# Optimization experiments

Measured on AMD Instinct MI355X. Metric: run time of the kernel, lower is better.

The kernel has to match this reference:

```python
import jax, jax.numpy as jnp
import numpy as np
from jax import lax

J2 = -1.0
J4 = 0.5
KT = 0.5
DT = 0.01
SIGMA = float(np.sqrt(2.0 * KT * DT))  # noise scale per Euler-Maruyama step


def setup_inputs() -> dict:
    key = jax.random.key(0)
    k_x, = jax.random.split(key, 1)
    n_samples, n_dim = 2048, 256
    x0 = jax.random.normal(k_x, (n_samples, n_dim), dtype=jnp.float32)
    b = jnp.zeros((n_dim,), dtype=jnp.float32)  # learned bias parameter
    return {"x0": x0, "b": b, "n_steps": 500}


def reference(x0, b, n_steps):
    # Langevin dynamics: x <- x - grad_V(x)*dt + sqrt(2 kT dt)*N(0,1)
    # grad_V(x) = 2*J2*x + 4*J4*x^3 + b
    keys = jax.random.split(jax.random.key(1), n_steps)

    def step(x, k):
        grad = 2.0 * J2 * x + 4.0 * J4 * x * x * x + b
        noise = jax.random.normal(k, x.shape, x.dtype) * SIGMA
        return x - grad * DT + noise, None

    x, _ = lax.scan(step, x0, keys)
    return x
```

## Files before the change

kernel.cpp:

```cpp
#include <hip/hip_runtime.h>


typedef float v2f __attribute__((ext_vector_type(2)));

__device__ __forceinline__ void tf2x32(unsigned k0, unsigned k1,
                                       unsigned c0, unsigned c1,
                                       unsigned& o0, unsigned& o1) {
  const unsigned k2 = k0 ^ k1 ^ 0x1BD11BDAu;
  unsigned x0 = c0 + k0, x1 = c1 + k1;
#define TF1(R) x0 += x1; x1 = ((x1 << (R)) | (x1 >> (32 - (R)))); x1 ^= x0;
  TF1(13) TF1(15) TF1(26) TF1(6)  x0 += k1; x1 += k2 + 1u;
  TF1(17) TF1(29) TF1(16) TF1(24) x0 += k2; x1 += k0 + 2u;
  TF1(13) TF1(15) TF1(26) TF1(6)  x0 += k0; x1 += k1 + 3u;
  TF1(17) TF1(29) TF1(16) TF1(24) x0 += k1; x1 += k2 + 4u;
  TF1(13) TF1(15) TF1(26) TF1(6)  x0 += k2; x1 += k0 + 5u;
#undef TF1
  o0 = x0; o1 = x1;
}

__device__ __forceinline__ void tf_fold2k(unsigned ka0, unsigned ka1,
                                          unsigned kb0, unsigned kb1,
                                          unsigned cj,
                                          unsigned& ra, unsigned& rb) {
  const unsigned ka2 = ka0 ^ ka1 ^ 0x1BD11BDAu;
  const unsigned kb2 = kb0 ^ kb1 ^ 0x1BD11BDAu;
  unsigned a0 = ka0, a1 = cj + ka1;
  unsigned b0 = kb0, b1 = cj + kb1;
#define TFR2(R)                                   \
  a0 += a1; b0 += b1;                             \
  a1 = ((a1 << (R)) | (a1 >> (32 - (R)))) ^ a0;   \
  b1 = ((b1 << (R)) | (b1 >> (32 - (R)))) ^ b0;
  TFR2(13) TFR2(15) TFR2(26) TFR2(6)
  a0 += ka1; b0 += kb1; a1 += ka2 + 1u; b1 += kb2 + 1u;
  TFR2(17) TFR2(29) TFR2(16) TFR2(24)
  a0 += ka2; b0 += kb2; a1 += ka0 + 2u; b1 += kb0 + 2u;
  TFR2(13) TFR2(15) TFR2(26) TFR2(6)
  a0 += ka0; b0 += kb0; a1 += ka1 + 3u; b1 += kb1 + 3u;
  TFR2(17) TFR2(29) TFR2(16) TFR2(24)
  a0 += ka1; b0 += kb1; a1 += ka2 + 4u; b1 += kb2 + 4u;
  TFR2(13) TFR2(15) TFR2(26) TFR2(6)
  a0 += ka2; b0 += kb2; a1 += ka0 + 5u; b1 += kb0 + 5u;
#undef TFR2
  ra = a0 ^ a1;
  rb = b0 ^ b1;
}

__device__ __forceinline__ void b2n2(unsigned bba, unsigned bbb,
                                     float& na, float& nb) {
  v2f f;
  f.x = __uint_as_float((bba >> 9) | 0x3F800000u) - 1.0f;
  f.y = __uint_as_float((bbb >> 9) | 0x3F800000u) - 1.0f;
  const v2f u = __builtin_elementwise_fma(f, (v2f)2.0f, (v2f)(-0.99999994f));
  const v2f m = u * u;
  const v2f tt = (v2f)1.0f - m;
  v2f l;
  l.x = __log2f(tt.x);
  l.y = __log2f(tt.y);
  const v2f w = l * (v2f)(-0.693147180559945f);
  const bool sa = w.x < 5.0f, sb = w.y < 5.0f;
  const v2f zc = w - (v2f)2.5f;
  v2f z;
  z.x = sa ? zc.x : (__builtin_amdgcn_sqrtf(w.x) - 3.0f);
  z.y = sb ? zc.y : (__builtin_amdgcn_sqrtf(w.y) - 3.0f);
#define SEL2(A, B) (v2f){sa ? (A) : (B), sb ? (A) : (B)}
  v2f p = SEL2(2.81022636e-08f, -0.000200214257f);
  p = __builtin_elementwise_fma(p, z, SEL2(3.43273939e-07f, 0.000100950558f));
  p = __builtin_elementwise_fma(p, z, SEL2(-3.5233877e-06f, 0.00134934322f));
  p = __builtin_elementwise_fma(p, z, SEL2(-4.39150654e-06f, -0.00367342844f));
  p = __builtin_elementwise_fma(p, z, SEL2(0.00021858087f, 0.00573950773f));
  p = __builtin_elementwise_fma(p, z, SEL2(-0.00125372503f, -0.0076224613f));
  p = __builtin_elementwise_fma(p, z, SEL2(-0.00417768164f, 0.00943887047f));
  p = __builtin_elementwise_fma(p, z, SEL2(0.246640727f, 1.00167406f));
  p = __builtin_elementwise_fma(p, z, SEL2(1.50140941f, 2.83297682f));
#undef SEL2
  const v2f n = (p * u) * (v2f)__uint_as_float(0x3FB504F3u);
  na = n.x;
  nb = n.y;
}

__global__ __launch_bounds__(128, 8) void langevin_tf(
    const float* __restrict__ x0p, const float* __restrict__ bias,
    const int* __restrict__ nsteps_p, float* __restrict__ out,
    int N, int ndim) {
  __shared__ __align__(16) unsigned skeys[512 * 2];
  const int n_steps = __builtin_amdgcn_readfirstlane(nsteps_p[0]);
  const int nfill = n_steps < 512 ? n_steps : 512;
  for (int l = (int)threadIdx.x; l < nfill; l += (int)blockDim.x) {
    unsigned o0, o1;
    tf2x32(0u, 1u, 0u, (unsigned)l, o0, o1);
    skeys[2 * l] = o0;
    skeys[2 * l + 1] = o1;
  }
  __syncthreads();

  const int j = (int)(blockIdx.x * blockDim.x + threadIdx.x);
  if (j >= N) return;
  const unsigned cj = (unsigned)j;
  float x = x0p[j];
  const float b = bias[j % ndim];

  if (n_steps <= 512) {
    const uint4* sk4 = (const uint4*)skeys;
    int t = 0;
#pragma unroll 1
    for (; t + 1 < n_steps; t += 2) {
      const uint4 kk = sk4[t >> 1];
      unsigned ra, rb;
      tf_fold2k(kk.x, kk.y, kk.z, kk.w, cj, ra, rb);
      float na, nb;
      b2n2(ra, rb, na, nb);
      float g = -2.0f * x + ((2.0f * x) * x) * x + b;
      x = (x - g * 0.01f) + na * 0.1f;
      g = -2.0f * x + ((2.0f * x) * x) * x + b;
      x = (x - g * 0.01f) + nb * 0.1f;
    }
    if (t < n_steps) {
      const unsigned o0 = skeys[2 * t], o1 = skeys[2 * t + 1];
      unsigned ra, rb;
      tf_fold2k(o0, o1, o0, o1, cj, ra, rb);
      float na, nb;
      b2n2(ra, ra, na, nb);
      const float g = -2.0f * x + ((2.0f * x) * x) * x + b;
      x = (x - g * 0.01f) + na * 0.1f;
    }
  } else {
    for (int t = 0; t < n_steps; t += 2) {
      unsigned oa0, oa1, ob0, ob1;
      tf2x32(0u, 1u, 0u, (unsigned)t, oa0, oa1);
      tf2x32(0u, 1u, 0u, (unsigned)(t + 1), ob0, ob1);
      unsigned ra, rb;
      tf_fold2k(oa0, oa1, ob0, ob1, cj, ra, rb);
      float na, nb;
      b2n2(ra, rb, na, nb);
      float g = -2.0f * x + ((2.0f * x) * x) * x + b;
      x = (x - g * 0.01f) + na * 0.1f;
      if (t + 1 < n_steps) {
        g = -2.0f * x + ((2.0f * x) * x) * x + b;
        x = (x - g * 0.01f) + nb * 0.1f;
      }
    }
  }
  out[j] = x;
}

extern "C" void kernel_launch(void* const* d_in, const int* in_sizes, int n_in,
                              void* d_out, int out_size, void* d_ws, size_t ws_size,
                              hipStream_t stream) {
  (void)n_in; (void)d_ws; (void)ws_size; (void)out_size;
  const float* x0 = (const float*)d_in[0];
  const float* b = (const float*)d_in[1];
  const int* ns = (const int*)d_in[2];
  float* out = (float*)d_out;

  const int n = in_sizes[0];
  const int ndim = in_sizes[1];
  const int block = 128;
  const int grid = (n + block - 1) / block;
  hipLaunchKernelGGL(langevin_tf, dim3(grid), dim3(block), 0, stream,
                     x0, b, ns, out, n, ndim);
}
```

Before: 681.6 us.

## Precompute key schedule, branch tail polynomial wave-uniformly, fold update into FMAs

Stores the third Threefry key word in the shared key table so it is not recomputed per step. The inverse-erf tail polynomial is now evaluated only when some lane in the wave needs it. The gradient update is folded into a chain of FMAs with scalarized constants, and the block size grows to 256. Dropping explicit packed v2f math and the small numeric reordering may cost packed-FMA throughput or add slight differences in rounding.

```diff
diff --git a/kernel.cpp b/kernel.cpp
--- a/kernel.cpp
+++ b/kernel.cpp
@@ -1,7 +1,9 @@
 #include <hip/hip_runtime.h>
 
 
-typedef float v2f __attribute__((ext_vector_type(2)));
+__device__ __forceinline__ float sconst(float v) {
+  return __uint_as_float(__builtin_amdgcn_readfirstlane(__float_as_uint(v)));
+}
 
 __device__ __forceinline__ void tf2x32(unsigned k0, unsigned k1,
                                        unsigned c0, unsigned c1,
@@ -18,78 +20,40 @@
   o0 = x0; o1 = x1;
 }
 
-__device__ __forceinline__ void tf_fold2k(unsigned ka0, unsigned ka1,
-                                          unsigned kb0, unsigned kb1,
-                                          unsigned cj,
+__device__ __forceinline__ void tf_fold2k(uint4 ka, uint4 kb, unsigned cj,
                                           unsigned& ra, unsigned& rb) {
-  const unsigned ka2 = ka0 ^ ka1 ^ 0x1BD11BDAu;
-  const unsigned kb2 = kb0 ^ kb1 ^ 0x1BD11BDAu;
-  unsigned a0 = ka0, a1 = cj + ka1;
-  unsigned b0 = kb0, b1 = cj + kb1;
+  unsigned a0 = ka.x, a1 = cj + ka.y;
+  unsigned b0 = kb.x, b1 = cj + kb.y;
 #define TFR2(R)                                   \
   a0 += a1; b0 += b1;                             \
   a1 = ((a1 << (R)) | (a1 >> (32 - (R)))) ^ a0;   \
   b1 = ((b1 << (R)) | (b1 >> (32 - (R)))) ^ b0;
   TFR2(13) TFR2(15) TFR2(26) TFR2(6)
-  a0 += ka1; b0 += kb1; a1 += ka2 + 1u; b1 += kb2 + 1u;
+  a0 += ka.y; b0 += kb.y; a1 = a1 + ka.z + 1u; b1 = b1 + kb.z + 1u;
   TFR2(17) TFR2(29) TFR2(16) TFR2(24)
-  a0 += ka2; b0 += kb2; a1 += ka0 + 2u; b1 += kb0 + 2u;
+  a0 += ka.z; b0 += kb.z; a1 = a1 + ka.x + 2u; b1 = b1 + kb.x + 2u;
   TFR2(13) TFR2(15) TFR2(26) TFR2(6)
-  a0 += ka0; b0 += kb0; a1 += ka1 + 3u; b1 += kb1 + 3u;
+  a0 += ka.x; b0 += kb.x; a1 = a1 + ka.y + 3u; b1 = b1 + kb.y + 3u;
   TFR2(17) TFR2(29) TFR2(16) TFR2(24)
-  a0 += ka1; b0 += kb1; a1 += ka2 + 4u; b1 += kb2 + 4u;
+  a0 += ka.y; b0 += kb.y; a1 = a1 + ka.z + 4u; b1 = b1 + kb.z + 4u;
   TFR2(13) TFR2(15) TFR2(26) TFR2(6)
-  a0 += ka2; b0 += kb2; a1 += ka0 + 5u; b1 += kb0 + 5u;
+  a0 += ka.z; b0 += kb.z; a1 = a1 + ka.x + 5u; b1 = b1 + kb.x + 5u;
 #undef TFR2
   ra = a0 ^ a1;
   rb = b0 ^ b1;
 }
 
-__device__ __forceinline__ void b2n2(unsigned bba, unsigned bbb,
-                                     float& na, float& nb) {
-  v2f f;
-  f.x = __uint_as_float((bba >> 9) | 0x3F800000u) - 1.0f;
-  f.y = __uint_as_float((bbb >> 9) | 0x3F800000u) - 1.0f;
-  const v2f u = __builtin_elementwise_fma(f, (v2f)2.0f, (v2f)(-0.99999994f));
-  const v2f m = u * u;
-  const v2f tt = (v2f)1.0f - m;
-  v2f l;
-  l.x = __log2f(tt.x);
-  l.y = __log2f(tt.y);
-  const v2f w = l * (v2f)(-0.693147180559945f);
-  const bool sa = w.x < 5.0f, sb = w.y < 5.0f;
-  const v2f zc = w - (v2f)2.5f;
-  v2f z;
-  z.x = sa ? zc.x : (__builtin_amdgcn_sqrtf(w.x) - 3.0f);
-  z.y = sb ? zc.y : (__builtin_amdgcn_sqrtf(w.y) - 3.0f);
-#define SEL2(A, B) (v2f){sa ? (A) : (B), sb ? (A) : (B)}
-  v2f p = SEL2(2.81022636e-08f, -0.000200214257f);
-  p = __builtin_elementwise_fma(p, z, SEL2(3.43273939e-07f, 0.000100950558f));
-  p = __builtin_elementwise_fma(p, z, SEL2(-3.5233877e-06f, 0.00134934322f));
-  p = __builtin_elementwise_fma(p, z, SEL2(-4.39150654e-06f, -0.00367342844f));
-  p = __builtin_elementwise_fma(p, z, SEL2(0.00021858087f, 0.00573950773f));
-  p = __builtin_elementwise_fma(p, z, SEL2(-0.00125372503f, -0.0076224613f));
-  p = __builtin_elementwise_fma(p, z, SEL2(-0.00417768164f, 0.00943887047f));
-  p = __builtin_elementwise_fma(p, z, SEL2(0.246640727f, 1.00167406f));
-  p = __builtin_elementwise_fma(p, z, SEL2(1.50140941f, 2.83297682f));
-#undef SEL2
-  const v2f n = (p * u) * (v2f)__uint_as_float(0x3FB504F3u);
-  na = n.x;
-  nb = n.y;
-}
-
-__global__ __launch_bounds__(128, 8) void langevin_tf(
+__global__ __launch_bounds__(256, 8) void langevin_tf(
     const float* __restrict__ x0p, const float* __restrict__ bias,
     const int* __restrict__ nsteps_p, float* __restrict__ out,
     int N, int ndim) {
-  __shared__ __align__(16) unsigned skeys[512 * 2];
+  __shared__ __align__(16) uint4 skeys[512];
   const int n_steps = __builtin_amdgcn_readfirstlane(nsteps_p[0]);
   const int nfill = n_steps < 512 ? n_steps : 512;
   for (int l = (int)threadIdx.x; l < nfill; l += (int)blockDim.x) {
     unsigned o0, o1;
     tf2x32(0u, 1u, 0u, (unsigned)l, o0, o1);
-    skeys[2 * l] = o0;
-    skeys[2 * l + 1] = o1;
+    skeys[l] = make_uint4(o0, o1, o0 ^ o1 ^ 0x1BD11BDAu, 0u);
   }
   __syncthreads();
 
@@ -99,45 +63,114 @@
   float x = x0p[j];
   const float b = bias[j % ndim];
 
+  const float LO = sconst(-0.99999994f);
+  const float NLN2 = sconst(-0.693147180559945f);
+  const float C8 = sconst(2.81022636e-08f), C7 = sconst(3.43273939e-07f);
+  const float C6 = sconst(-3.5233877e-06f), C5 = sconst(-4.39150654e-06f);
+  const float C4 = sconst(0.00021858087f),  C3 = sconst(-0.00125372503f);
+  const float C2 = sconst(-0.00417768164f), C1 = sconst(0.246640727f);
+  const float C0 = sconst(1.50140941f);
+  const float T8 = sconst(-0.000200214257f), T7 = sconst(0.000100950558f);
+  const float T6 = sconst(0.00134934322f),   T5 = sconst(-0.00367342844f);
+  const float T4 = sconst(0.00573950773f),   T3 = sconst(-0.0076224613f);
+  const float T2 = sconst(0.00943887047f),   T1 = sconst(1.00167406f);
+  const float T0 = sconst(2.83297682f);
+  const float CS = sconst(0.1f * __uint_as_float(0x3FB504F3u));
+  const float A1 = sconst(1.02f);
+  const float A3 = sconst(-0.02f);
+  const float bp = b * -0.01f;
+
   if (n_steps <= 512) {
-    const uint4* sk4 = (const uint4*)skeys;
     int t = 0;
 #pragma unroll 1
     for (; t + 1 < n_steps; t += 2) {
-      const uint4 kk = sk4[t >> 1];
+      const uint4 ka = skeys[t];
+      const uint4 kb = skeys[t + 1];
       unsigned ra, rb;
-      tf_fold2k(kk.x, kk.y, kk.z, kk.w, cj, ra, rb);
-      float na, nb;
-      b2n2(ra, rb, na, nb);
-      float g = -2.0f * x + ((2.0f * x) * x) * x + b;
-      x = (x - g * 0.01f) + na * 0.1f;
-      g = -2.0f * x + ((2.0f * x) * x) * x + b;
-      x = (x - g * 0.01f) + nb * 0.1f;
+      tf_fold2k(ka, kb, cj, ra, rb);
+      const float fa = __uint_as_float((ra >> 9) | 0x3F800000u) - 1.0f;
+      const float fb = __uint_as_float((rb >> 9) | 0x3F800000u) - 1.0f;
+      const float ua = fmaf(fa, 2.0f, LO);
+      const float ub = fmaf(fb, 2.0f, LO);
+      const float wa = __log2f(1.0f - ua * ua) * NLN2;
+      const float wb = __log2f(1.0f - ub * ub) * NLN2;
+      const float za = wa - 2.5f;
+      const float zb = wb - 2.5f;
+      float pa = C8, pb = C8;
+      pa = fmaf(pa, za, C7); pb = fmaf(pb, zb, C7);
+      pa = fmaf(pa, za, C6); pb = fmaf(pb, zb, C6);
+      pa = fmaf(pa, za, C5); pb = fmaf(pb, zb, C5);
+      pa = fmaf(pa, za, C4); pb = fmaf(pb, zb, C4);
+      pa = fmaf(pa, za, C3); pb = fmaf(pb, zb, C3);
+      pa = fmaf(pa, za, C2); pb = fmaf(pb, zb, C2);
+      pa = fmaf(pa, za, C1); pb = fmaf(pb, zb, C1);
+      pa = fmaf(pa, za, C0); pb = fmaf(pb, zb, C0);
+      float ea = pa * ua;
+      float eb = pb * ub;
+      if (__any((wa >= 5.0f) | (wb >= 5.0f))) {
+        const float qza = __builtin_amdgcn_sqrtf(wa) - 3.0f;
+        const float qzb = __builtin_amdgcn_sqrtf(wb) - 3.0f;
+        float qa = T8, qb = T8;
+        qa = fmaf(qa, qza, T7); qb = fmaf(qb, qzb, T7);
+        qa = fmaf(qa, qza, T6); qb = fmaf(qb, qzb, T6);
+        qa = fmaf(qa, qza, T5); qb = fmaf(qb, qzb, T5);
+        qa = fmaf(qa, qza, T4); qb = fmaf(qb, qzb, T4);
+        qa = fmaf(qa, qza, T3); qb = fmaf(qb, qzb, T3);
+        qa = fmaf(qa, qza, T2); qb = fmaf(qb, qzb, T2);
+        qa = fmaf(qa, qza, T1); qb = fmaf(qb, qzb, T1);
+        qa = fmaf(qa, qza, T0); qb = fmaf(qb, qzb, T0);
+        ea = (wa >= 5.0f) ? qa * ua : ea;
+        eb = (wb >= 5.0f) ? qb * ub : eb;
+      }
+      float x3 = (x * x) * x;
+      x = fmaf(x, A1, fmaf(x3, A3, fmaf(ea, CS, bp)));
+      x3 = (x * x) * x;
+      x = fmaf(x, A1, fmaf(x3, A3, fmaf(eb, CS, bp)));
     }
     if (t < n_steps) {
-      const unsigned o0 = skeys[2 * t], o1 = skeys[2 * t + 1];
+      const uint4 ka = skeys[t];
       unsigned ra, rb;
-      tf_fold2k(o0, o1, o0, o1, cj, ra, rb);
-      float na, nb;
-      b2n2(ra, ra, na, nb);
-      const float g = -2.0f * x + ((2.0f * x) * x) * x + b;
-      x = (x - g * 0.01f) + na * 0.1f;
+      tf_fold2k(ka, ka, cj, ra, rb);
+      const float fa = __uint_as_float((ra >> 9) | 0x3F800000u) - 1.0f;
+      const float ua = fmaf(fa, 2.0f, LO);
+      const float wa = __log2f(1.0f - ua * ua) * NLN2;
+      float pa, za;
+      if (wa < 5.0f) { za = wa - 2.5f;
+        pa = C8; pa = fmaf(pa, za, C7); pa = fmaf(pa, za, C6);
+        pa = fmaf(pa, za, C5); pa = fmaf(pa, za, C4); pa = fmaf(pa, za, C3);
+        pa = fmaf(pa, za, C2); pa = fmaf(pa, za, C1); pa = fmaf(pa, za, C0);
+      } else { za = __builtin_amdgcn_sqrtf(wa) - 3.0f;
+        pa = T8; pa = fmaf(pa, za, T7); pa = fmaf(pa, za, T6);
+        pa = fmaf(pa, za, T5); pa = fmaf(pa, za, T4); pa = fmaf(pa, za, T3);
+        pa = fmaf(pa, za, T2); pa = fmaf(pa, za, T1); pa = fmaf(pa, za, T0);
+      }
+      const float ea = pa * ua;
+      const float x3 = (x * x) * x;
+      x = fmaf(x, A1, fmaf(x3, A3, fmaf(ea, CS, bp)));
     }
   } else {
-    for (int t = 0; t < n_steps; t += 2) {
-      unsigned oa0, oa1, ob0, ob1;
-      tf2x32(0u, 1u, 0u, (unsigned)t, oa0, oa1);
-      tf2x32(0u, 1u, 0u, (unsigned)(t + 1), ob0, ob1);
+    for (int t = 0; t < n_steps; ++t) {
+      unsigned o0, o1;
+      tf2x32(0u, 1u, 0u, (unsigned)t, o0, o1);
+      const uint4 ka = make_uint4(o0, o1, o0 ^ o1 ^ 0x1BD11BDAu, 0u);
       unsigned ra, rb;
-      tf_fold2k(oa0, oa1, ob0, ob1, cj, ra, rb);
-      float na, nb;
-      b2n2(ra, rb, na, nb);
-      float g = -2.0f * x + ((2.0f * x) * x) * x + b;
-      x = (x - g * 0.01f) + na * 0.1f;
-      if (t + 1 < n_steps) {
-        g = -2.0f * x + ((2.0f * x) * x) * x + b;
-        x = (x - g * 0.01f) + nb * 0.1f;
+      tf_fold2k(ka, ka, cj, ra, rb);
+      const float fa = __uint_as_float((ra >> 9) | 0x3F800000u) - 1.0f;
+      const float ua = fmaf(fa, 2.0f, LO);
+      const float wa = __log2f(1.0f - ua * ua) * NLN2;
+      float pa, za;
+      if (wa < 5.0f) { za = wa - 2.5f;
+        pa = C8; pa = fmaf(pa, za, C7); pa = fmaf(pa, za, C6);
+        pa = fmaf(pa, za, C5); pa = fmaf(pa, za, C4); pa = fmaf(pa, za, C3);
+        pa = fmaf(pa, za, C2); pa = fmaf(pa, za, C1); pa = fmaf(pa, za, C0);
+      } else { za = __builtin_amdgcn_sqrtf(wa) - 3.0f;
+        pa = T8; pa = fmaf(pa, za, T7); pa = fmaf(pa, za, T6);
+        pa = fmaf(pa, za, T5); pa = fmaf(pa, za, T4); pa = fmaf(pa, za, T3);
+        pa = fmaf(pa, za, T2); pa = fmaf(pa, za, T1); pa = fmaf(pa, za, T0);
       }
+      const float ea = pa * ua;
+      const float x3 = (x * x) * x;
+      x = fmaf(x, A1, fmaf(x3, A3, fmaf(ea, CS, bp)));
     }
   }
   out[j] = x;
@@ -154,7 +187,7 @@
 
   const int n = in_sizes[0];
   const int ndim = in_sizes[1];
-  const int block = 128;
+  const int block = 256;
   const int grid = (n + block - 1) / block;
   hipLaunchKernelGGL(langevin_tf, dim3(grid), dim3(block), 0, stream,
                      x0, b, ns, out, n, ndim);
```

Result: faster. 573.5 us (-15.9%).
